# Kernel optimization log

Measured on AMD Instinct MI355X. Metric: run time of the kernel, lower is better.

## Reference

```python
import jax, jax.numpy as jnp
import numpy as np

N_NODES = 100000
N_EDGES = 1600000
IN_FEATS = 128
N_HIDDEN = 128
N_CLASSES = 47


def _glorot(key, shape):
    lim = float(np.sqrt(6.0 / (shape[0] + shape[1])))
    return jax.random.uniform(key, shape, jnp.float32, -lim, lim)


def setup_inputs() -> dict:
    key = jax.random.key(0)
    ks = jax.random.split(key, 9)
    x = jax.random.normal(ks[0], (N_NODES, IN_FEATS), jnp.float32)
    src = jax.random.randint(ks[1], (N_EDGES,), 0, N_NODES, jnp.int32)
    dst = jax.random.randint(ks[2], (N_EDGES,), 0, N_NODES, jnp.int32)
    return {
        "x": x,
        "W_self_0": _glorot(ks[3], (IN_FEATS, N_HIDDEN)),
        "W_neigh_0": _glorot(ks[4], (IN_FEATS, N_HIDDEN)),
        "W_self_1": _glorot(ks[5], (N_HIDDEN, N_HIDDEN)),
        "W_neigh_1": _glorot(ks[6], (N_HIDDEN, N_HIDDEN)),
        "W_self_2": _glorot(ks[7], (N_HIDDEN, N_CLASSES)),
        "W_neigh_2": _glorot(ks[8], (N_HIDDEN, N_CLASSES)),
        "src": src,
        "dst": dst,
    }


def _sage_layer(h, src, dst, W_self, W_neigh):
    # mean aggregation of in-neighbor features (DGL SAGEConv 'mean', no bias)
    neigh_sum = jax.ops.segment_sum(h[src], dst, num_segments=N_NODES)  # [N, d]
    deg = jax.ops.segment_sum(jnp.ones((src.shape[0],), h.dtype), dst,
                              num_segments=N_NODES)  # [N]
    h_neigh = neigh_sum / jnp.maximum(deg, 1.0)[:, None]
    return h @ W_self + h_neigh @ W_neigh


def reference(x, W_self_0, W_neigh_0, W_self_1, W_neigh_1, W_self_2, W_neigh_2,
              src, dst):
    h = _sage_layer(x, src, dst, W_self_0, W_neigh_0)
    h = jax.nn.relu(h)  # dropout is identity in eval/reference mode
    h = _sage_layer(h, src, dst, W_self_1, W_neigh_1)
    h = jax.nn.relu(h)
    h = _sage_layer(h, src, dst, W_self_2, W_neigh_2)
    return h
```

## Files before the change

### kernel.cpp

```cpp
#include <hip/hip_runtime.h>
#include <hip/hip_bf16.h>

#define NN 100000
#define NE 1600000
#define NBK 391
#define SLOT 4608

typedef __attribute__((ext_vector_type(8))) short bf16x8;
typedef __attribute__((ext_vector_type(4))) float f32x4;

__device__ __forceinline__ unsigned short f2bf(float x) {
    unsigned u = __float_as_uint(x);
    return (unsigned short)((u + 0x7fffu + ((u >> 16) & 1u)) >> 16);
}
__device__ __forceinline__ float bflo(unsigned v) { return __uint_as_float(v << 16); }
__device__ __forceinline__ float bfhi(unsigned v) { return __uint_as_float(v & 0xffff0000u); }

#define ACCV(A, v) do { \
    A[0] += bflo((v).x); A[1] += bfhi((v).x); \
    A[2] += bflo((v).y); A[3] += bfhi((v).y); \
    A[4] += bflo((v).z); A[5] += bfhi((v).z); \
    A[6] += bflo((v).w); A[7] += bfhi((v).w); } while (0)

__device__ __forceinline__ int swz8(int i, int nwg) {
    int q = nwg >> 3, r = nwg & 7;
    int x = i & 7, j = i >> 3;
    return (x < r) ? x * (q + 1) + j : r * (q + 1) + (x - r) * q + j;
}

__global__ __launch_bounds__(256) void cast_x(const float* __restrict__ x,
                                              unsigned short* __restrict__ h,
                                              int* __restrict__ gcur) {
    if (blockIdx.x == 0) {
        for (int i = threadIdx.x; i < NBK; i += 256) gcur[i * 16] = i * SLOT;
    }
    int chunk = swz8(blockIdx.x, (int)gridDim.x);
    int i = (chunk * 256 + (int)threadIdx.x) * 4;
    if (i >= NN * 128) return;
    float4 v = *(const float4*)(x + i);
    unsigned out0 = ((unsigned)f2bf(v.y) << 16) | f2bf(v.x);
    unsigned out1 = ((unsigned)f2bf(v.w) << 16) | f2bf(v.z);
    *(uint2*)(h + i) = make_uint2(out0, out1);
}

__global__ __launch_bounds__(256) void sort_scatter(const int* __restrict__ src,
                                                    const int* __restrict__ dst,
                                                    int* __restrict__ gcur,
                                                    unsigned* __restrict__ pairs) {
    __shared__ int bcnt[NBK], gbase[NBK], lcur[NBK];
    int t = threadIdx.x;
    for (int i = t; i < NBK; i += 256) { bcnt[i] = 0; lcur[i] = 0; }
    __syncthreads();
    int base = blockIdx.x * 2048;
    int d[8];
#pragma unroll
    for (int i = 0; i < 8; ++i) {
        int e = base + t + i * 256;
        d[i] = (e < NE) ? dst[e] : -1;
        if (d[i] >= 0) atomicAdd(&bcnt[d[i] >> 8], 1);
    }
    __syncthreads();
    for (int i = t; i < NBK; i += 256)
        if (bcnt[i]) gbase[i] = atomicAdd(&gcur[i * 16], bcnt[i]);
    __syncthreads();
#pragma unroll
    for (int i = 0; i < 8; ++i) {
        if (d[i] >= 0) {
            int e = base + t + i * 256;
            int b = d[i] >> 8;
            int p = atomicAdd(&lcur[b], 1);
            pairs[gbase[b] + p] = ((unsigned)src[e] << 8) | (unsigned)(d[i] & 255);
        }
    }
}

__global__ __launch_bounds__(512) void scan_pack(const int* __restrict__ gcur, int* __restrict__ bbase,
                                                 int* __restrict__ row_ptr,
                                                 const float* __restrict__ Ws0, const float* __restrict__ Wn0,
                                                 const float* __restrict__ Ws1, const float* __restrict__ Wn1,
                                                 const float* __restrict__ Ws2, const float* __restrict__ Wn2,
                                                 unsigned short* __restrict__ wp0, unsigned short* __restrict__ wp1,
                                                 unsigned short* __restrict__ wp2) {
    int t = threadIdx.x;
    if (blockIdx.x == 0) {
        __shared__ int s[512];
        int v = (t < NBK) ? (gcur[t * 16] - t * SLOT) : 0;
        s[t] = v;
        __syncthreads();
        for (int off = 1; off < 512; off <<= 1) {
            int u = (t >= off) ? s[t - off] : 0;
            __syncthreads();
            s[t] += u;
            __syncthreads();
        }
        int ex = s[t] - v;
        if (t <= NBK) bbase[t] = ex;
        if (t == 0) row_ptr[NN] = NE;
        return;
    }
    int local = (blockIdx.x - 1) * 512 + t;
    const float *Ws, *Wn;
    unsigned short* wp;
    int Ncols, NF;
    if (local < 32768)      { Ws = Ws0; Wn = Wn0; wp = wp0; Ncols = 128; NF = 8; }
    else if (local < 65536) { Ws = Ws1; Wn = Wn1; wp = wp1; Ncols = 128; NF = 8; local -= 32768; }
    else                    { Ws = Ws2; Wn = Wn2; wp = wp2; Ncols = 47;  NF = 3; local -= 65536; }
    int j = local & 7;
    int lane = (local >> 3) & 63;
    int fid = local >> 9;
    int nf = fid % NF;
    int kstep = fid / NF;
    int k = kstep * 32 + (lane >> 4) * 8 + j;
    int n = nf * 16 + (lane & 15);
    float v = 0.f;
    if (n < Ncols) v = (k < 128) ? Ws[k * Ncols + n] : Wn[(k - 128) * Ncols + n];
    wp[local] = f2bf(v);
}

__global__ __launch_bounds__(256) void bucket_place(const unsigned* __restrict__ pairs,
                                                    const int* __restrict__ bbase,
                                                    int* __restrict__ row_ptr,
                                                    float* __restrict__ inv_deg,
                                                    int* __restrict__ csr) {
    __shared__ int hist[256], sc[256], cur[256];
    int b = blockIdx.x, t = threadIdx.x;
    hist[t] = 0;
    __syncthreads();
    int pbeg = b * SLOT;
    int beg = bbase[b];
    int cnt = bbase[b + 1] - beg;
    for (int i = t; i < cnt; i += 256) atomicAdd(&hist[pairs[pbeg + i] & 255u], 1);
    __syncthreads();
    int deg = hist[t];
    sc[t] = deg;
    __syncthreads();
    for (int off = 1; off < 256; off <<= 1) {
        int u = (t >= off) ? sc[t - off] : 0;
        __syncthreads();
        sc[t] += u;
        __syncthreads();
    }
    int ex = sc[t] - deg;
    int node = b * 256 + t;
    if (node < NN) {
        row_ptr[node] = beg + ex;
        inv_deg[node] = 1.0f / (float)max(deg, 1);
    }
    cur[t] = beg + ex;
    __syncthreads();
    for (int i = t; i < cnt; i += 256) {
        unsigned p = pairs[pbeg + i];
        int pos = atomicAdd(&cur[p & 255u], 1);
        csr[pos] = (int)(p & 0xFFFFFF00u);
    }
}

__global__ __launch_bounds__(256) void aggregate(const unsigned* __restrict__ h32,
                                                 const int* __restrict__ csr,
                                                 const int* __restrict__ row_ptr,
                                                 const float* __restrict__ inv_deg,
                                                 unsigned* __restrict__ agg32) {
    int lane = threadIdx.x & 63;
    int wave = threadIdx.x >> 6;
    int chunk = (blockIdx.x & 7) * 3125 + (blockIdx.x >> 3);
    int node = chunk * 4 + wave;
    int g = lane >> 4;
    unsigned l16 = (unsigned)(lane & 15) * 16;
    const char* hb = (const char*)h32;
    int beg = row_ptr[node], end = row_ptr[node + 1];
    float inv = inv_deg[node];
    float acc[8];
#pragma unroll
    for (int j = 0; j < 8; ++j) acc[j] = 0.f;

    int e = beg;
    for (; e + 15 < end; e += 16) {
        int c0 = csr[e + g];
        int c1 = csr[e + 4 + g];
        int c2 = csr[e + 8 + g];
        int c3 = csr[e + 12 + g];
        uint4 v0 = *(const uint4*)(hb + (unsigned)c0 + l16);
        uint4 v1 = *(const uint4*)(hb + (unsigned)c1 + l16);
        uint4 v2 = *(const uint4*)(hb + (unsigned)c2 + l16);
        uint4 v3 = *(const uint4*)(hb + (unsigned)c3 + l16);
        ACCV(acc, v0); ACCV(acc, v1); ACCV(acc, v2); ACCV(acc, v3);
    }
    for (; e + 3 < end; e += 4) {
        int c = csr[e + g];
        uint4 v = *(const uint4*)(hb + (unsigned)c + l16);
        ACCV(acc, v);
    }
    int rem = end - e;
    if (g < rem) {
        int c = csr[e + g];
        uint4 v = *(const uint4*)(hb + (unsigned)c + l16);
        ACCV(acc, v);
    }

#pragma unroll
    for (int j = 0; j < 8; ++j) {
        acc[j] += __shfl_xor(acc[j], 16, 64);
        acc[j] += __shfl_xor(acc[j], 32, 64);
    }
    if (lane < 16) {
        unsigned d0 = ((unsigned)f2bf(acc[1] * inv) << 16) | f2bf(acc[0] * inv);
        unsigned d1 = ((unsigned)f2bf(acc[3] * inv) << 16) | f2bf(acc[2] * inv);
        unsigned d2 = ((unsigned)f2bf(acc[5] * inv) << 16) | f2bf(acc[4] * inv);
        unsigned d3 = ((unsigned)f2bf(acc[7] * inv) << 16) | f2bf(acc[6] * inv);
        *(uint4*)((char*)agg32 + (size_t)node * 256 + l16) = make_uint4(d0, d1, d2, d3);
    }
}

template <int NF, bool LAST>
__global__ __launch_bounds__(256) void gemm_k(const unsigned short* __restrict__ hA,
                                              const unsigned short* __restrict__ hAgg,
                                              const unsigned short* __restrict__ wpack,
                                              unsigned short* __restrict__ hOut,
                                              float* __restrict__ fOut) {
    int lane = threadIdx.x & 63;
    int wave = threadIdx.x >> 6;
    int chunk = swz8(blockIdx.x, (int)gridDim.x);
    int base = chunk * 64;
    int aRow = base + wave * 16 + (lane & 15);
    int kgrp = (lane >> 4) * 8;

    f32x4 acc[NF];
#pragma unroll
    for (int f = 0; f < NF; ++f)
#pragma unroll
        for (int q = 0; q < 4; ++q) acc[f][q] = 0.f;

    bool inb = (aRow < NN);
#pragma unroll
    for (int half = 0; half < 2; ++half) {
        const unsigned short* A = half ? hAgg : hA;
#pragma unroll
        for (int ks = 0; ks < 4; ++ks) {
            bf16x8 afrag;
            if (inb) {
                afrag = *(const bf16x8*)(A + (size_t)aRow * 128 + ks * 32 + kgrp);
            } else {
#pragma unroll
                for (int j = 0; j < 8; ++j) afrag[j] = 0;
            }
            int kstep = half * 4 + ks;
#pragma unroll
            for (int nf = 0; nf < NF; ++nf) {
                bf16x8 b = *(const bf16x8*)(wpack + (((kstep * NF + nf) * 64) + lane) * 8);
                acc[nf] = __builtin_amdgcn_mfma_f32_16x16x32_bf16(afrag, b, acc[nf], 0, 0, 0);
            }
        }
    }

    int col0 = lane & 15;
    int rBase = base + wave * 16 + (lane >> 4) * 4;
#pragma unroll
    for (int nf = 0; nf < NF; ++nf) {
        int col = nf * 16 + col0;
        if (LAST) {
            if (col < 47) {
#pragma unroll
                for (int q = 0; q < 4; ++q) {
                    int row = rBase + q;
                    if (row < NN) fOut[(size_t)row * 47 + col] = acc[nf][q];
                }
            }
        } else {
#pragma unroll
            for (int q = 0; q < 4; ++q) {
                int row = rBase + q;
                if (row < NN) hOut[(size_t)row * 128 + col] = f2bf(fmaxf(acc[nf][q], 0.f));
            }
        }
    }
}

static inline size_t alignup(size_t x) { return (x + 255) & ~(size_t)255; }

extern "C" void kernel_launch(void* const* d_in, const int* in_sizes, int n_in,
                              void* d_out, int out_size, void* d_ws, size_t ws_size,
                              hipStream_t stream) {
    const float* x   = (const float*)d_in[0];
    const float* Ws0 = (const float*)d_in[1];
    const float* Wn0 = (const float*)d_in[2];
    const float* Ws1 = (const float*)d_in[3];
    const float* Wn1 = (const float*)d_in[4];
    const float* Ws2 = (const float*)d_in[5];
    const float* Wn2 = (const float*)d_in[6];
    const int* src   = (const int*)d_in[7];
    const int* dst   = (const int*)d_in[8];
    float* out = (float*)d_out;

    char* w = (char*)d_ws;
    size_t off = 0;
    int* row_ptr   = (int*)(w + off);   off += alignup((NN + 1) * 4);
    int* bbase     = (int*)(w + off);   off += alignup((NBK + 1) * 4);
    int* gcur      = (int*)(w + off);   off += alignup((size_t)NBK * 16 * 4);
    float* inv_deg = (float*)(w + off); off += alignup(NN * 4);
    int* csr       = (int*)(w + off);   off += alignup((size_t)NE * 4);
    unsigned* pairs = (unsigned*)(w + off); off += alignup((size_t)NBK * SLOT * 4);
    unsigned short* wp0 = (unsigned short*)(w + off); off += alignup(8 * 8 * 64 * 8 * 2);
    unsigned short* wp1 = (unsigned short*)(w + off); off += alignup(8 * 8 * 64 * 8 * 2);
    unsigned short* wp2 = (unsigned short*)(w + off); off += alignup(8 * 3 * 64 * 8 * 2);
    unsigned short* hA  = (unsigned short*)(w + off); off += alignup((size_t)NN * 128 * 2);
    unsigned short* hB  = (unsigned short*)(w + off); off += alignup((size_t)NN * 128 * 2);
    unsigned short* agg = (unsigned short*)(w + off); off += alignup((size_t)NN * 128 * 2);

    cast_x<<<dim3((NN * 128 / 4 + 255) / 256), dim3(256), 0, stream>>>(x, hA, gcur);
    sort_scatter<<<dim3((NE + 2047) / 2048), dim3(256), 0, stream>>>(src, dst, gcur, pairs);
    scan_pack<<<dim3(153), dim3(512), 0, stream>>>(gcur, bbase, row_ptr,
                                                   Ws0, Wn0, Ws1, Wn1, Ws2, Wn2, wp0, wp1, wp2);
    bucket_place<<<dim3(NBK), dim3(256), 0, stream>>>(pairs, bbase, row_ptr, inv_deg, csr);

    const int aggGrid  = NN / 4;
    const int gemmGrid = (NN + 63) / 64;

    aggregate<<<dim3(aggGrid), dim3(256), 0, stream>>>((const unsigned*)hA, csr, row_ptr, inv_deg, (unsigned*)agg);
    gemm_k<8, false><<<dim3(gemmGrid), dim3(256), 0, stream>>>(hA, agg, wp0, hB, nullptr);
    aggregate<<<dim3(aggGrid), dim3(256), 0, stream>>>((const unsigned*)hB, csr, row_ptr, inv_deg, (unsigned*)agg);
    gemm_k<8, false><<<dim3(gemmGrid), dim3(256), 0, stream>>>(hB, agg, wp1, hA, nullptr);
    aggregate<<<dim3(aggGrid), dim3(256), 0, stream>>>((const unsigned*)hA, csr, row_ptr, inv_deg, (unsigned*)agg);
    gemm_k<3, true><<<dim3(gemmGrid), dim3(256), 0, stream>>>(hA, agg, wp2, nullptr, out);
}
```

Baseline: 322.4 us.

## Fold weight packing into cast kernel and bucket scan into placement

Merges weight packing into the x-cast kernel and drops the separate scan kernel. Each bucket_place block now computes its own bucket base by summing the preceding bucket counts read from gcur. This removes one kernel launch and its serialization point, at the cost of redundant per-block prefix work. The aggregate accumulators are also switched to float2 vectors to encourage packed adds.

After: 322.0 us. No clear change (-0.1%).

```diff
diff --git a/kernel.cpp b/kernel.cpp
--- a/kernel.cpp
+++ b/kernel.cpp
@@ -8,19 +8,20 @@
 
 typedef __attribute__((ext_vector_type(8))) short bf16x8;
 typedef __attribute__((ext_vector_type(4))) float f32x4;
+typedef __attribute__((ext_vector_type(2))) float f32x2;
 
 __device__ __forceinline__ unsigned short f2bf(float x) {
     unsigned u = __float_as_uint(x);
     return (unsigned short)((u + 0x7fffu + ((u >> 16) & 1u)) >> 16);
 }
-__device__ __forceinline__ float bflo(unsigned v) { return __uint_as_float(v << 16); }
-__device__ __forceinline__ float bfhi(unsigned v) { return __uint_as_float(v & 0xffff0000u); }
-
-#define ACCV(A, v) do { \
-    A[0] += bflo((v).x); A[1] += bfhi((v).x); \
-    A[2] += bflo((v).y); A[3] += bfhi((v).y); \
-    A[4] += bflo((v).z); A[5] += bfhi((v).z); \
-    A[6] += bflo((v).w); A[7] += bfhi((v).w); } while (0)
+__device__ __forceinline__ f32x2 up2(unsigned v) {
+    f32x2 r;
+    r[0] = __uint_as_float(v << 16);
+    r[1] = __uint_as_float(v & 0xffff0000u);
+    return r;
+}
+#define ACC2(A, v) do { \
+    A[0] += up2((v).x); A[1] += up2((v).y); A[2] += up2((v).z); A[3] += up2((v).w); } while (0)
 
 __device__ __forceinline__ int swz8(int i, int nwg) {
     int q = nwg >> 3, r = nwg & 7;
@@ -28,77 +29,29 @@
     return (x < r) ? x * (q + 1) + j : r * (q + 1) + (x - r) * q + j;
 }
 
-__global__ __launch_bounds__(256) void cast_x(const float* __restrict__ x,
-                                              unsigned short* __restrict__ h,
-                                              int* __restrict__ gcur) {
-    if (blockIdx.x == 0) {
+__global__ __launch_bounds__(256) void prep(const float* __restrict__ x,
+                                            unsigned short* __restrict__ h,
+                                            int* __restrict__ gcur,
+                                            const float* __restrict__ Ws0, const float* __restrict__ Wn0,
+                                            const float* __restrict__ Ws1, const float* __restrict__ Wn1,
+                                            const float* __restrict__ Ws2, const float* __restrict__ Wn2,
+                                            unsigned short* __restrict__ wp0, unsigned short* __restrict__ wp1,
+                                            unsigned short* __restrict__ wp2) {
+    int b = blockIdx.x;
+    if (b < 12500) {
+        int chunk = swz8(b, 12500);
+        int i = (chunk * 256 + (int)threadIdx.x) * 4;
+        float4 v = *(const float4*)(x + i);
+        unsigned out0 = ((unsigned)f2bf(v.y) << 16) | f2bf(v.x);
+        unsigned out1 = ((unsigned)f2bf(v.w) << 16) | f2bf(v.z);
+        *(uint2*)(h + i) = make_uint2(out0, out1);
+        return;
+    }
+    int pb = b - 12500;
+    if (pb == 0) {
         for (int i = threadIdx.x; i < NBK; i += 256) gcur[i * 16] = i * SLOT;
     }
-    int chunk = swz8(blockIdx.x, (int)gridDim.x);
-    int i = (chunk * 256 + (int)threadIdx.x) * 4;
-    if (i >= NN * 128) return;
-    float4 v = *(const float4*)(x + i);
-    unsigned out0 = ((unsigned)f2bf(v.y) << 16) | f2bf(v.x);
-    unsigned out1 = ((unsigned)f2bf(v.w) << 16) | f2bf(v.z);
-    *(uint2*)(h + i) = make_uint2(out0, out1);
-}
-
-__global__ __launch_bounds__(256) void sort_scatter(const int* __restrict__ src,
-                                                    const int* __restrict__ dst,
-                                                    int* __restrict__ gcur,
-                                                    unsigned* __restrict__ pairs) {
-    __shared__ int bcnt[NBK], gbase[NBK], lcur[NBK];
-    int t = threadIdx.x;
-    for (int i = t; i < NBK; i += 256) { bcnt[i] = 0; lcur[i] = 0; }
-    __syncthreads();
-    int base = blockIdx.x * 2048;
-    int d[8];
-#pragma unroll
-    for (int i = 0; i < 8; ++i) {
-        int e = base + t + i * 256;
-        d[i] = (e < NE) ? dst[e] : -1;
-        if (d[i] >= 0) atomicAdd(&bcnt[d[i] >> 8], 1);
-    }
-    __syncthreads();
-    for (int i = t; i < NBK; i += 256)
-        if (bcnt[i]) gbase[i] = atomicAdd(&gcur[i * 16], bcnt[i]);
-    __syncthreads();
-#pragma unroll
-    for (int i = 0; i < 8; ++i) {
-        if (d[i] >= 0) {
-            int e = base + t + i * 256;
-            int b = d[i] >> 8;
-            int p = atomicAdd(&lcur[b], 1);
-            pairs[gbase[b] + p] = ((unsigned)src[e] << 8) | (unsigned)(d[i] & 255);
-        }
-    }
-}
-
-__global__ __launch_bounds__(512) void scan_pack(const int* __restrict__ gcur, int* __restrict__ bbase,
-                                                 int* __restrict__ row_ptr,
-                                                 const float* __restrict__ Ws0, const float* __restrict__ Wn0,
-                                                 const float* __restrict__ Ws1, const float* __restrict__ Wn1,
-                                                 const float* __restrict__ Ws2, const float* __restrict__ Wn2,
-                                                 unsigned short* __restrict__ wp0, unsigned short* __restrict__ wp1,
-                                                 unsigned short* __restrict__ wp2) {
-    int t = threadIdx.x;
-    if (blockIdx.x == 0) {
-        __shared__ int s[512];
-        int v = (t < NBK) ? (gcur[t * 16] - t * SLOT) : 0;
-        s[t] = v;
-        __syncthreads();
-        for (int off = 1; off < 512; off <<= 1) {
-            int u = (t >= off) ? s[t - off] : 0;
-            __syncthreads();
-            s[t] += u;
-            __syncthreads();
-        }
-        int ex = s[t] - v;
-        if (t <= NBK) bbase[t] = ex;
-        if (t == 0) row_ptr[NN] = NE;
-        return;
-    }
-    int local = (blockIdx.x - 1) * 512 + t;
+    int local = pb * 256 + (int)threadIdx.x;
     const float *Ws, *Wn;
     unsigned short* wp;
     int Ncols, NF;
@@ -117,18 +70,60 @@
     wp[local] = f2bf(v);
 }
 
+__global__ __launch_bounds__(256) void sort_scatter(const int* __restrict__ src,
+                                                    const int* __restrict__ dst,
+                                                    int* __restrict__ gcur,
+                                                    unsigned* __restrict__ pairs) {
+    __shared__ int bcnt[NBK], gbase[NBK], lcur[NBK];
+    int t = threadIdx.x;
+    for (int i = t; i < NBK; i += 256) { bcnt[i] = 0; lcur[i] = 0; }
+    __syncthreads();
+    int base = blockIdx.x * 2048;
+    int d[8];
+#pragma unroll
+    for (int i = 0; i < 8; ++i) {
+        int e = base + t + i * 256;
+        d[i] = (e < NE) ? dst[e] : -1;
+        if (d[i] >= 0) atomicAdd(&bcnt[d[i] >> 8], 1);
+    }
+    __syncthreads();
+    for (int i = t; i < NBK; i += 256)
+        if (bcnt[i]) gbase[i] = atomicAdd(&gcur[i * 16], bcnt[i]);
+    __syncthreads();
+#pragma unroll
+    for (int i = 0; i < 8; ++i) {
+        if (d[i] >= 0) {
+            int e = base + t + i * 256;
+            int b = d[i] >> 8;
+            int p = atomicAdd(&lcur[b], 1);
+            pairs[gbase[b] + p] = ((unsigned)src[e] << 8) | (unsigned)(d[i] & 255);
+        }
+    }
+}
+
 __global__ __launch_bounds__(256) void bucket_place(const unsigned* __restrict__ pairs,
-                                                    const int* __restrict__ bbase,
+                                                    const int* __restrict__ gcur,
                                                     int* __restrict__ row_ptr,
                                                     float* __restrict__ inv_deg,
                                                     int* __restrict__ csr) {
+    __shared__ int cnts[NBK];
+    __shared__ int red[256];
     __shared__ int hist[256], sc[256], cur[256];
     int b = blockIdx.x, t = threadIdx.x;
+    for (int i = t; i < NBK; i += 256) cnts[i] = gcur[i * 16] - i * SLOT;
     hist[t] = 0;
     __syncthreads();
+    int part = 0;
+    for (int i = t; i < b; i += 256) part += cnts[i];
+    red[t] = part;
+    __syncthreads();
+    for (int off = 128; off > 0; off >>= 1) {
+        if (t < off) red[t] += red[t + off];
+        __syncthreads();
+    }
+    int beg = red[0];
+    int cnt = cnts[b];
     int pbeg = b * SLOT;
-    int beg = bbase[b];
-    int cnt = bbase[b + 1] - beg;
     for (int i = t; i < cnt; i += 256) atomicAdd(&hist[pairs[pbeg + i] & 255u], 1);
     __syncthreads();
     int deg = hist[t];
@@ -146,6 +141,7 @@
         row_ptr[node] = beg + ex;
         inv_deg[node] = 1.0f / (float)max(deg, 1);
     }
+    if (b == NBK - 1 && t == 0) row_ptr[NN] = beg + cnt;
     cur[t] = beg + ex;
     __syncthreads();
     for (int i = t; i < cnt; i += 256) {
@@ -169,9 +165,9 @@
     const char* hb = (const char*)h32;
     int beg = row_ptr[node], end = row_ptr[node + 1];
     float inv = inv_deg[node];
-    float acc[8];
-#pragma unroll
-    for (int j = 0; j < 8; ++j) acc[j] = 0.f;
+    f32x2 acc[4];
+#pragma unroll
+    for (int j = 0; j < 4; ++j) { acc[j][0] = 0.f; acc[j][1] = 0.f; }
 
     int e = beg;
     for (; e + 15 < end; e += 16) {
@@ -183,30 +179,35 @@
         uint4 v1 = *(const uint4*)(hb + (unsigned)c1 + l16);
         uint4 v2 = *(const uint4*)(hb + (unsigned)c2 + l16);
         uint4 v3 = *(const uint4*)(hb + (unsigned)c3 + l16);
-        ACCV(acc, v0); ACCV(acc, v1); ACCV(acc, v2); ACCV(acc, v3);
+        ACC2(acc, v0); ACC2(acc, v1); ACC2(acc, v2); ACC2(acc, v3);
     }
     for (; e + 3 < end; e += 4) {
         int c = csr[e + g];
         uint4 v = *(const uint4*)(hb + (unsigned)c + l16);
-        ACCV(acc, v);
+        ACC2(acc, v);
     }
     int rem = end - e;
     if (g < rem) {
         int c = csr[e + g];
         uint4 v = *(const uint4*)(hb + (unsigned)c + l16);
-        ACCV(acc, v);
-    }
-
-#pragma unroll
-    for (int j = 0; j < 8; ++j) {
-        acc[j] += __shfl_xor(acc[j], 16, 64);
-        acc[j] += __shfl_xor(acc[j], 32, 64);
+        ACC2(acc, v);
+    }
+
+#pragma unroll
+    for (int j = 0; j < 4; ++j) {
+#pragma unroll
+        for (int k = 0; k < 2; ++k) {
+            float s = acc[j][k];
+            s += __shfl_xor(s, 16, 64);
+            s += __shfl_xor(s, 32, 64);
+            acc[j][k] = s;
+        }
     }
     if (lane < 16) {
-        unsigned d0 = ((unsigned)f2bf(acc[1] * inv) << 16) | f2bf(acc[0] * inv);
-        unsigned d1 = ((unsigned)f2bf(acc[3] * inv) << 16) | f2bf(acc[2] * inv);
-        unsigned d2 = ((unsigned)f2bf(acc[5] * inv) << 16) | f2bf(acc[4] * inv);
-        unsigned d3 = ((unsigned)f2bf(acc[7] * inv) << 16) | f2bf(acc[6] * inv);
+        unsigned d0 = ((unsigned)f2bf(acc[0][1] * inv) << 16) | f2bf(acc[0][0] * inv);
+        unsigned d1 = ((unsigned)f2bf(acc[1][1] * inv) << 16) | f2bf(acc[1][0] * inv);
+        unsigned d2 = ((unsigned)f2bf(acc[2][1] * inv) << 16) | f2bf(acc[2][0] * inv);
+        unsigned d3 = ((unsigned)f2bf(acc[3][1] * inv) << 16) | f2bf(acc[3][0] * inv);
         *(uint4*)((char*)agg32 + (size_t)node * 256 + l16) = make_uint4(d0, d1, d2, d3);
     }
 }
@@ -294,7 +295,6 @@
     char* w = (char*)d_ws;
     size_t off = 0;
     int* row_ptr   = (int*)(w + off);   off += alignup((NN + 1) * 4);
-    int* bbase     = (int*)(w + off);   off += alignup((NBK + 1) * 4);
     int* gcur      = (int*)(w + off);   off += alignup((size_t)NBK * 16 * 4);
     float* inv_deg = (float*)(w + off); off += alignup(NN * 4);
     int* csr       = (int*)(w + off);   off += alignup((size_t)NE * 4);
@@ -306,11 +306,10 @@
     unsigned short* hB  = (unsigned short*)(w + off); off += alignup((size_t)NN * 128 * 2);
     unsigned short* agg = (unsigned short*)(w + off); off += alignup((size_t)NN * 128 * 2);
 
-    cast_x<<<dim3((NN * 128 / 4 + 255) / 256), dim3(256), 0, stream>>>(x, hA, gcur);
+    prep<<<dim3(12804), dim3(256), 0, stream>>>(x, hA, gcur,
+                                                Ws0, Wn0, Ws1, Wn1, Ws2, Wn2, wp0, wp1, wp2);
     sort_scatter<<<dim3((NE + 2047) / 2048), dim3(256), 0, stream>>>(src, dst, gcur, pairs);
-    scan_pack<<<dim3(153), dim3(512), 0, stream>>>(gcur, bbase, row_ptr,
-                                                   Ws0, Wn0, Ws1, Wn1, Ws2, Wn2, wp0, wp1, wp2);
-    bucket_place<<<dim3(NBK), dim3(256), 0, stream>>>(pairs, bbase, row_ptr, inv_deg, csr);
+    bucket_place<<<dim3(NBK), dim3(256), 0, stream>>>(pairs, gcur, row_ptr, inv_deg, csr);
 
     const int aggGrid  = NN / 4;
     const int gemmGrid = (NN + 63) / 64;
```
